# Performance work log

Hardware: AMD Instinct MI355X
Metric: run time of the kernel (lower is better)

Reference implementation:

```python
import jax, jax.numpy as jnp
import numpy as np

D_MODEL = 1024
NHEAD = 16
D_K = D_MODEL // NHEAD
EPS = 1e-5


def _layernorm(x, scale, bias):
    m = jnp.mean(x, axis=-1, keepdims=True)
    v = jnp.var(x, axis=-1, keepdims=True)
    return (x - m) * jax.lax.rsqrt(v + EPS) * scale + bias


def setup_inputs() -> dict:
    key = jax.random.key(0)
    ks = jax.random.split(key, 16)
    d, h = D_MODEL, 4 * D_MODEL
    s = 1.0 / np.sqrt(d)
    inp = {
        "x": jax.random.normal(ks[0], (2, 2048, d), dtype=jnp.float32),
        "Wq": jax.random.normal(ks[1], (d, d), dtype=jnp.float32) * s,
        "bq": jnp.zeros((d,), jnp.float32),
        "Wk": jax.random.normal(ks[2], (d, d), dtype=jnp.float32) * s,
        "bk": jnp.zeros((d,), jnp.float32),
        "Wv": jax.random.normal(ks[3], (d, d), dtype=jnp.float32) * s,
        "bv": jnp.zeros((d,), jnp.float32),
        "Wo": jax.random.normal(ks[4], (d, d), dtype=jnp.float32) * s,
        "bo": jnp.zeros((d,), jnp.float32),
        "ln1_scale": jnp.ones((d,), jnp.float32),
        "ln1_bias": jnp.zeros((d,), jnp.float32),
        "ln2_scale": jnp.ones((d,), jnp.float32),
        "ln2_bias": jnp.zeros((d,), jnp.float32),
        "W1": jax.random.normal(ks[5], (d, h), dtype=jnp.float32) * s,
        "b1": jnp.zeros((h,), jnp.float32),
        "W2": jax.random.normal(ks[6], (h, d), dtype=jnp.float32) * (1.0 / np.sqrt(h)),
        "b2": jnp.zeros((d,), jnp.float32),
    }
    return inp


def reference(x, Wq, bq, Wk, bk, Wv, bv, Wo, bo,
              ln1_scale, ln1_bias, ln2_scale, ln2_bias,
              W1, b1, W2, b2):
    batch, seq, d_model = x.shape
    # Faithful to original: q is viewed WITHOUT transpose (asymmetric vs k,v)
    q = (x @ Wq + bq).reshape(batch, NHEAD, seq, D_K)
    k = (x @ Wk + bk).reshape(batch, seq, NHEAD, D_K).transpose(0, 2, 1, 3)
    v = (x @ Wv + bv).reshape(batch, seq, NHEAD, D_K).transpose(0, 2, 1, 3)
    # scores: [B, H, S, S]
    scores = jnp.einsum('bhqd,bhkd->bhqk', q, k) / np.sqrt(D_K)
    attn = jax.nn.softmax(scores, axis=-1)
    o = jnp.einsum('bhqk,bhkd->bhqd', attn, v)  # [B,H,S,dk]
    o = o.transpose(0, 2, 1, 3).reshape(batch, seq, d_model)
    x = _layernorm(x + o @ Wo + bo, ln1_scale, ln1_bias)
    ff = jax.nn.relu(x @ W1 + b1) @ W2 + b2
    x = _layernorm(x + ff, ln2_scale, ln2_bias)
    return x
```

## Files before the change

### kernel.cpp

```cpp
#include <hip/hip_runtime.h>
#include <cstdint>

typedef __bf16 bf16x8 __attribute__((ext_vector_type(8)));
typedef float  floatx4 __attribute__((ext_vector_type(4)));

__device__ __forceinline__ unsigned short f2bf(float x) {
  union { float f; uint32_t u; } v; v.f = x;
  uint32_t r = (v.u + 0x7FFFu + ((v.u >> 16) & 1u)) >> 16;
  return (unsigned short)r;
}

__device__ __forceinline__ void async_copy16(const void* g, void* l) {
  __builtin_amdgcn_global_load_lds(
      (const __attribute__((address_space(1))) uint32_t*)g,
      (__attribute__((address_space(3))) uint32_t*)l, 16, 0, 0);
}

template<int OUT_BF16, int RELU>
__global__ __launch_bounds__(256, 2)
void gemm_bt_kernel(const unsigned short* __restrict__ A,
                    const unsigned short* __restrict__ Bt,
                    void* __restrict__ C, const float* __restrict__ bias,
                    int M, int N, int K, int Kper) {
  __shared__ __align__(16) unsigned short lA[128 * 32];
  __shared__ __align__(16) unsigned short lB[128 * 32];
  const int tid  = threadIdx.x;
  const int wave = tid >> 6;
  const int lane = tid & 63;

  const int gx = gridDim.x, gy = gridDim.y;
  int flat = blockIdx.y * gx + blockIdx.x;
  const int per = (gx * gy) >> 3;
  flat = (flat & 7) * per + (flat >> 3);
  const int sq = flat >> 6, inner = flat & 63;
  const int sqm = gy >> 3;
  const int m0 = ((sq % sqm) * 8 + (inner & 7)) * 128;
  const int n0 = ((sq / sqm) * 8 + (inner >> 3)) * 128;

  const int kz = blockIdx.z;
  const int wm = (wave >> 1) * 64;
  const int wn = (wave & 1) * 64;
  const int sa_row = lane >> 2;
  const int sa_k   = ((lane & 3) ^ ((lane >> 3) & 3)) * 8;
  const int fr = lane & 15;
  const int fq = lane >> 4;
  const int sw = (fr >> 1) & 3;

  floatx4 acc[4][4];
  #pragma unroll
  for (int i = 0; i < 4; ++i)
    #pragma unroll
    for (int j = 0; j < 4; ++j)
      acc[i][j] = (floatx4){0.f, 0.f, 0.f, 0.f};

  const int kIters = Kper >> 5;
  for (int kt = 0; kt < kIters; ++kt) {
    const int k0 = kz * Kper + (kt << 5);
    __syncthreads();
    #pragma unroll
    for (int j = 0; j < 2; ++j) {
      const int chunk = wave * 2 + j;
      const int row   = chunk * 16 + sa_row;
      async_copy16(A  + (size_t)(m0 + row) * K + (k0 + sa_k), &lA[chunk * 512]);
      async_copy16(Bt + (size_t)(n0 + row) * K + (k0 + sa_k), &lB[chunk * 512]);
    }
    asm volatile("s_waitcnt vmcnt(0)" ::: "memory");
    __syncthreads();
    bf16x8 af[4], bf[4];
    #pragma unroll
    for (int t = 0; t < 4; ++t) {
      af[t] = *(const bf16x8*)&lA[(wm + t * 16 + fr) * 32 + (fq ^ sw) * 8];
      bf[t] = *(const bf16x8*)&lB[(wn + t * 16 + fr) * 32 + (fq ^ sw) * 8];
    }
    #pragma unroll
    for (int mt = 0; mt < 4; ++mt)
      #pragma unroll
      for (int nt = 0; nt < 4; ++nt)
        acc[mt][nt] = __builtin_amdgcn_mfma_f32_16x16x32_bf16(af[mt], bf[nt], acc[mt][nt], 0, 0, 0);
  }

  const float* bp = (kz == 0) ? bias : nullptr;
  char* Cz = (char*)C + (size_t)kz * M * N * (OUT_BF16 ? 2 : 4);
  #pragma unroll
  for (int mt = 0; mt < 4; ++mt) {
    #pragma unroll
    for (int nt = 0; nt < 4; ++nt) {
      const int gn = n0 + wn + nt * 16 + fr;
      const float bv = bp ? bp[gn] : 0.f;
      #pragma unroll
      for (int r = 0; r < 4; ++r) {
        const int gm = m0 + wm + mt * 16 + fq * 4 + r;
        float v = acc[mt][nt][r] + bv;
        if (RELU) v = fmaxf(v, 0.f);
        if (OUT_BF16) ((unsigned short*)Cz)[(size_t)gm * N + gn] = f2bf(v);
        else          ((float*)Cz)[(size_t)gm * N + gn] = v;
      }
    }
  }
}

__global__ __launch_bounds__(256)
void repack_v_kernel(const unsigned short* __restrict__ X,
                     unsigned short* __restrict__ Vt) {
  const int bid = blockIdx.x;
  const int st = bid & 31, h = (bid >> 5) & 15, b = bid >> 9;
  const int bh = b * 16 + h;
  const int s0 = st * 64;
  const int t = threadIdx.x;
  const int sl = t >> 2;
  const int c  = (t & 3) * 16;
  __shared__ __align__(16) unsigned short vt[64][72];
  {
    const uint4* srcV = (const uint4*)(X + (size_t)(b * 2048 + s0 + sl) * 3072 + 2048 + h * 64 + c);
    uint4* dstL = (uint4*)&vt[sl][c];
    dstL[0] = srcV[0]; dstL[1] = srcV[1];
  }
  __syncthreads();
  const int d = t >> 2, c0 = (t & 3) * 16;
  unsigned short tmp[16];
  #pragma unroll
  for (int j = 0; j < 16; ++j) {
    const int chat = c0 + j;
    const int key = (chat & 3) * 16 + (chat >> 2);
    tmp[j] = vt[key][d];
  }
  uint4* dstV = (uint4*)(Vt + ((size_t)bh * 64 + d) * 2048 + s0 + c0);
  dstV[0] = *(uint4*)&tmp[0];
  dstV[1] = *(uint4*)&tmp[8];
}

__global__ __launch_bounds__(256, 4)
void flash_attn_kernel(const unsigned short* __restrict__ QKVb,
                       const unsigned short* __restrict__ Vt,
                       float* __restrict__ Opart, float* __restrict__ Lpart) {
  const int bid = blockIdx.x;
  const int qt = bid & 15, h = (bid >> 4) & 15, b = (bid >> 8) & 1, ksp = bid >> 9;
  const int bh = b * 16 + h;
  const int wave = threadIdx.x >> 6, lane = threadIdx.x & 63;
  const int fr = lane & 15, fq = lane >> 4;

  __shared__ __align__(16) unsigned short lK[64 * 64];
  __shared__ __align__(16) unsigned short lV[64 * 64];
  __shared__ __align__(16) unsigned short lP[4][32 * 72];

  const int q_base = qt * 128 + wave * 32;
  bf16x8 aq[2][2];
  #pragma unroll
  for (int g = 0; g < 2; ++g) {
    const int s2 = q_base + g * 16 + fr;
    const unsigned short* qp = QKVb + (size_t)(b * 2048 + h * 128 + (s2 >> 4)) * 3072
                             + (s2 & 15) * 64 + fq * 8;
    aq[g][0] = *(const bf16x8*)qp;
    aq[g][1] = *(const bf16x8*)(qp + 32);
  }
  floatx4 o_acc[2][4];
  #pragma unroll
  for (int g = 0; g < 2; ++g)
    #pragma unroll
    for (int nt = 0; nt < 4; ++nt) o_acc[g][nt] = (floatx4){0.f, 0.f, 0.f, 0.f};
  float lrow[2][4];
  #pragma unroll
  for (int g = 0; g < 2; ++g)
    #pragma unroll
    for (int r = 0; r < 4; ++r) lrow[g][r] = 0.f;

  const unsigned short* Kg = QKVb + 1024 + h * 64;
  const unsigned short* Vg = Vt + (size_t)bh * 64 * 2048;

  const int srow = lane >> 3;
  const int scol = ((lane & 7) ^ (lane >> 3)) * 8;
  const int sw = fr & 7;

  for (int kt = ksp * 16; kt < ksp * 16 + 16; ++kt) {
    __syncthreads();
    #pragma unroll
    for (int j = 0; j < 2; ++j) {
      const int ch = wave * 2 + j;
      const int krow = ch * 8 + srow;
      async_copy16(Kg + (size_t)(b * 2048 + kt * 64 + krow) * 3072 + scol, (char*)lK + ch * 1024);
      async_copy16(Vg + (size_t)krow * 2048 + kt * 64 + scol, (char*)lV + ch * 1024);
    }
    asm volatile("s_waitcnt vmcnt(0)" ::: "memory");
    __syncthreads();

    floatx4 s_acc[2][4];
    #pragma unroll
    for (int nt = 0; nt < 4; ++nt) {
      const int row = (nt * 16 + fr) * 64;
      bf16x8 bk0 = *(const bf16x8*)&lK[row + ((0 + fq) ^ sw) * 8];
      bf16x8 bk1 = *(const bf16x8*)&lK[row + ((4 + fq) ^ sw) * 8];
      #pragma unroll
      for (int g = 0; g < 2; ++g) {
        floatx4 acc = (floatx4){0.f, 0.f, 0.f, 0.f};
        acc = __builtin_amdgcn_mfma_f32_16x16x32_bf16(aq[g][0], bk0, acc, 0, 0, 0);
        acc = __builtin_amdgcn_mfma_f32_16x16x32_bf16(aq[g][1], bk1, acc, 0, 0, 0);
        s_acc[g][nt] = acc;
      }
    }
    #pragma unroll
    for (int g = 0; g < 2; ++g) {
      #pragma unroll
      for (int r = 0; r < 4; ++r) {
        const float p0 = __builtin_amdgcn_exp2f(s_acc[g][0][r] * 0.18033688f);
        const float p1 = __builtin_amdgcn_exp2f(s_acc[g][1][r] * 0.18033688f);
        const float p2 = __builtin_amdgcn_exp2f(s_acc[g][2][r] * 0.18033688f);
        const float p3 = __builtin_amdgcn_exp2f(s_acc[g][3][r] * 0.18033688f);
        lrow[g][r] += (p0 + p1) + (p2 + p3);
        union { float f; uint32_t u; } c0, c1, c2, c3;
        c0.f = p0; c1.f = p1; c2.f = p2; c3.f = p3;
        uint2 pk;
        pk.x = (c1.u & 0xffff0000u) | (c0.u >> 16);
        pk.y = (c3.u & 0xffff0000u) | (c2.u >> 16);
        *(uint2*)&lP[wave][(g * 16 + fq * 4 + r) * 72 + fr * 4] = pk;
      }
    }
    #pragma unroll
    for (int g = 0; g < 2; ++g) {
      #pragma unroll
      for (int kk = 0; kk < 2; ++kk) {
        bf16x8 ap = *(const bf16x8*)&lP[wave][(g * 16 + fr) * 72 + kk * 32 + fq * 8];
        #pragma unroll
        for (int nt = 0; nt < 4; ++nt) {
          bf16x8 bv = *(const bf16x8*)&lV[(nt * 16 + fr) * 64 + ((kk * 4 + fq) ^ sw) * 8];
          o_acc[g][nt] = __builtin_amdgcn_mfma_f32_16x16x32_bf16(ap, bv, o_acc[g][nt], 0, 0, 0);
        }
      }
    }
  }

  const size_t rbase = (size_t)ksp * 65536 + (size_t)bh * 2048 + q_base;
  #pragma unroll
  for (int g = 0; g < 2; ++g) {
    #pragma unroll
    for (int r = 0; r < 4; ++r) {
      float l = lrow[g][r];
      #pragma unroll
      for (int off = 1; off < 16; off <<= 1) l += __shfl_xor(l, off);
      if (fr == 0) Lpart[rbase + g * 16 + fq * 4 + r] = l;
    }
    #pragma unroll
    for (int nt = 0; nt < 4; ++nt)
      #pragma unroll
      for (int r = 0; r < 4; ++r)
        Opart[(rbase + g * 16 + fq * 4 + r) * 64 + nt * 16 + fr] = o_acc[g][nt][r];
  }
}

__global__ __launch_bounds__(256)
void attn_combine_kernel(const float* __restrict__ Opart, const float* __restrict__ Lpart,
                         unsigned short* __restrict__ O) {
  const int i = blockIdx.x * 256 + threadIdx.x;
  const int row = i >> 4;
  const int d4 = (i & 15) * 4;
  const float4 o0 = *(const float4*)&Opart[(size_t)row * 64 + d4];
  const float4 o1 = *(const float4*)&Opart[(size_t)(row + 65536) * 64 + d4];
  const float inv = 1.f / (Lpart[row] + Lpart[row + 65536]);
  const int bq = ((row >> 15) << 11) | (row & 2047);
  const int h = (row >> 11) & 15;
  ushort4 r;
  r.x = f2bf((o0.x + o1.x) * inv);
  r.y = f2bf((o0.y + o1.y) * inv);
  r.z = f2bf((o0.z + o1.z) * inv);
  r.w = f2bf((o0.w + o1.w) * inv);
  *(ushort4*)&O[(size_t)bq * 1024 + h * 64 + d4] = r;
}

__global__ __launch_bounds__(256)
void ln_kernel(const float* __restrict__ X, const float* __restrict__ R,
               const float* __restrict__ R2,
               const float* __restrict__ sc, const float* __restrict__ bi,
               float* __restrict__ outF, unsigned short* __restrict__ outB) {
  const int row = blockIdx.x;
  const int t = threadIdx.x;
  const size_t base = (size_t)row * 1024 + t * 4;
  float4 a  = *(const float4*)&X[base];
  const float4 rv = *(const float4*)&R[base];
  const float4 r2 = *(const float4*)&R2[base];
  a.x += rv.x + r2.x; a.y += rv.y + r2.y; a.z += rv.z + r2.z; a.w += rv.w + r2.w;
  float sum = (a.x + a.y) + (a.z + a.w);
  float sq  = (a.x * a.x + a.y * a.y) + (a.z * a.z + a.w * a.w);
  #pragma unroll
  for (int off = 32; off > 0; off >>= 1) {
    sum += __shfl_down(sum, off);
    sq  += __shfl_down(sq, off);
  }
  __shared__ float s1[4], s2a[4];
  const int wave = t >> 6, lane = t & 63;
  if (lane == 0) { s1[wave] = sum; s2a[wave] = sq; }
  __syncthreads();
  sum = (s1[0] + s1[1]) + (s1[2] + s1[3]);
  sq  = (s2a[0] + s2a[1]) + (s2a[2] + s2a[3]);
  const float mean = sum * (1.f / 1024.f);
  const float var  = sq * (1.f / 1024.f) - mean * mean;
  const float rstd = rsqrtf(var + 1e-5f);
  const float4 s = *(const float4*)&sc[t * 4];
  const float4 bb = *(const float4*)&bi[t * 4];
  float4 y;
  y.x = (a.x - mean) * rstd * s.x + bb.x;
  y.y = (a.y - mean) * rstd * s.y + bb.y;
  y.z = (a.z - mean) * rstd * s.z + bb.z;
  y.w = (a.w - mean) * rstd * s.w + bb.w;
  if (outF) *(float4*)&outF[base] = y;
  if (outB) {
    ushort4 ob; ob.x = f2bf(y.x); ob.y = f2bf(y.y); ob.z = f2bf(y.z); ob.w = f2bf(y.w);
    *(ushort4*)&outB[base] = ob;
  }
}

__global__ void transpose_all_kernel(const float* __restrict__ Wq, const float* __restrict__ Wk,
                                     const float* __restrict__ Wv, const float* __restrict__ Wo,
                                     const float* __restrict__ W1, const float* __restrict__ W2,
                                     unsigned short* __restrict__ Wqkvt, unsigned short* __restrict__ Wot,
                                     unsigned short* __restrict__ W1t, unsigned short* __restrict__ W2t) {
  const int id = blockIdx.x;
  const float* W; unsigned short* Wt; int K, N, tile;
  if (id < 4096) {
    const int w = id >> 10; tile = id & 1023; K = 1024; N = 1024;
    if (w == 0)      { W = Wq; Wt = Wqkvt; }
    else if (w == 1) { W = Wk; Wt = Wqkvt + 1024 * 1024; }
    else if (w == 2) { W = Wv; Wt = Wqkvt + 2048 * 1024; }
    else             { W = Wo; Wt = Wot; }
  } else if (id < 8192) { tile = id - 4096; W = W1; Wt = W1t; K = 1024; N = 4096; }
  else                  { tile = id - 8192; W = W2; Wt = W2t; K = 4096; N = 1024; }
  const int tilesX = N >> 5;
  const int bx = (tile & (tilesX - 1)) * 32;
  const int by = (tile / tilesX) * 32;
  __shared__ float tl[32][33];
  const int tx = threadIdx.x, ty = threadIdx.y;
  #pragma unroll
  for (int i = ty; i < 32; i += 8)
    tl[i][tx] = W[(size_t)(by + i) * N + bx + tx];
  __syncthreads();
  #pragma unroll
  for (int i = ty; i < 32; i += 8)
    Wt[(size_t)(bx + i) * K + by + tx] = f2bf(tl[tx][i]);
}

__global__ void cast_bf16_kernel(const float* __restrict__ in,
                                 unsigned short* __restrict__ out, int n4) {
  const int i = blockIdx.x * 256 + threadIdx.x;
  if (i < n4) {
    float4 v = ((const float4*)in)[i];
    ushort4 o;
    o.x = f2bf(v.x); o.y = f2bf(v.y); o.z = f2bf(v.z); o.w = f2bf(v.w);
    ((ushort4*)out)[i] = o;
  }
}

__global__ void concat3_kernel(const float* __restrict__ a, const float* __restrict__ b,
                               const float* __restrict__ c, float* __restrict__ out) {
  int i = blockIdx.x * 256 + threadIdx.x;
  if (i < 1024) out[i] = a[i];
  else if (i < 2048) out[i] = b[i - 1024];
  else if (i < 3072) out[i] = c[i - 2048];
}

extern "C" void kernel_launch(void* const* d_in, const int* in_sizes, int n_in,
                              void* d_out, int out_size, void* d_ws, size_t ws_size,
                              hipStream_t stream) {
  const float* x    = (const float*)d_in[0];
  const float* Wq   = (const float*)d_in[1];
  const float* bq   = (const float*)d_in[2];
  const float* Wk   = (const float*)d_in[3];
  const float* bk   = (const float*)d_in[4];
  const float* Wv   = (const float*)d_in[5];
  const float* bv   = (const float*)d_in[6];
  const float* Wo   = (const float*)d_in[7];
  const float* bo   = (const float*)d_in[8];
  const float* ln1s = (const float*)d_in[9];
  const float* ln1b = (const float*)d_in[10];
  const float* ln2s = (const float*)d_in[11];
  const float* ln2b = (const float*)d_in[12];
  const float* W1   = (const float*)d_in[13];
  const float* b1   = (const float*)d_in[14];
  const float* W2   = (const float*)d_in[15];
  const float* b2   = (const float*)d_in[16];
  float* out = (float*)d_out;

  char* ws = (char*)d_ws;
  const size_t MB = 1u << 20;
  unsigned short* QKVb = (unsigned short*)(ws + 0);
  float*          t1   = (float*)(ws + 0);
  unsigned short* ffh  = (unsigned short*)(ws + 0);
  unsigned short* Vt   = (unsigned short*)(ws + 32 * MB);
  unsigned short* Ob   = (unsigned short*)(ws + 40 * MB);
  float*          ff   = (float*)(ws + 32 * MB);
  float*          Opart= (float*)(ws + 48 * MB);
  unsigned short* xb   = (unsigned short*)(ws + 48 * MB);
  unsigned short* Wqkvt= (unsigned short*)(ws + 56 * MB);
  float*          x1   = (float*)(ws + 64 * MB);
  float*          Lpart= (float*)(ws + 80 * MB);
  unsigned short* Wot  = (unsigned short*)(ws + 81 * MB);
  unsigned short* W1t  = (unsigned short*)(ws + 83 * MB);
  unsigned short* W2t  = (unsigned short*)(ws + 91 * MB);
  float*          bqkv = (float*)(ws + 99 * MB);
  unsigned short* x1b  = (unsigned short*)(ws + 100 * MB);

  cast_bf16_kernel<<<4096, 256, 0, stream>>>(x, xb, 1048576);
  transpose_all_kernel<<<12288, dim3(32, 8), 0, stream>>>(Wq, Wk, Wv, Wo, W1, W2,
                                                          Wqkvt, Wot, W1t, W2t);
  concat3_kernel<<<12, 256, 0, stream>>>(bq, bk, bv, bqkv);

  gemm_bt_kernel<1, 0><<<dim3(24, 32, 1), 256, 0, stream>>>(xb, Wqkvt, QKVb, bqkv, 4096, 3072, 1024, 1024);
  repack_v_kernel<<<1024, 256, 0, stream>>>(QKVb, Vt);
  flash_attn_kernel<<<1024, 256, 0, stream>>>(QKVb, Vt, Opart, Lpart);
  attn_combine_kernel<<<4096, 256, 0, stream>>>(Opart, Lpart, Ob);
  gemm_bt_kernel<0, 0><<<dim3(8, 32, 2), 256, 0, stream>>>(Ob, Wot, t1, bo, 4096, 1024, 1024, 512);
  ln_kernel<<<4096, 256, 0, stream>>>(x, t1, t1 + 4096 * 1024, ln1s, ln1b, x1, x1b);
  gemm_bt_kernel<1, 1><<<dim3(32, 32, 1), 256, 0, stream>>>(x1b, W1t, ffh, b1, 4096, 4096, 1024, 1024);
  gemm_bt_kernel<0, 0><<<dim3(8, 32, 2), 256, 0, stream>>>(ffh, W2t, ff, b2, 4096, 1024, 4096, 2048);
  ln_kernel<<<4096, 256, 0, stream>>>(x1, ff, ff + 4096 * 1024, ln2s, ln2b, out, nullptr);

  (void)in_sizes; (void)n_in; (void)out_size; (void)ws_size;
}
```

Before: 370.5 us.

## Double-buffer LDS tiles in GEMM to overlap async global loads with MFMA

Adds a second pair of LDS buffers to the bf16 GEMM so the next K-tile is prefetched via global_load_lds while the current tile feeds the MFMAs. Partial vmcnt waits and raw s_barrier replace the full drain and __syncthreads each iteration. It also precomputes the per-thread row pointers. The cost is double the LDS per block, which may limit occupancy, and the loop assumes an even kIters.

```diff
diff --git a/kernel.cpp b/kernel.cpp
--- a/kernel.cpp
+++ b/kernel.cpp
@@ -22,8 +22,10 @@
                     const unsigned short* __restrict__ Bt,
                     void* __restrict__ C, const float* __restrict__ bias,
                     int M, int N, int K, int Kper) {
-  __shared__ __align__(16) unsigned short lA[128 * 32];
-  __shared__ __align__(16) unsigned short lB[128 * 32];
+  __shared__ __align__(16) unsigned short l0A[128 * 32];
+  __shared__ __align__(16) unsigned short l0B[128 * 32];
+  __shared__ __align__(16) unsigned short l1A[128 * 32];
+  __shared__ __align__(16) unsigned short l1B[128 * 32];
   const int tid  = threadIdx.x;
   const int wave = tid >> 6;
   const int lane = tid & 63;
@@ -46,6 +48,13 @@
   const int fq = lane >> 4;
   const int sw = (fr >> 1) & 3;
 
+  const int r0 = (wave * 2 + 0) * 16 + sa_row;
+  const int r1 = (wave * 2 + 1) * 16 + sa_row;
+  const unsigned short* A0 = A  + (size_t)(m0 + r0) * K + kz * Kper + sa_k;
+  const unsigned short* A1 = A  + (size_t)(m0 + r1) * K + kz * Kper + sa_k;
+  const unsigned short* B0 = Bt + (size_t)(n0 + r0) * K + kz * Kper + sa_k;
+  const unsigned short* B1 = Bt + (size_t)(n0 + r1) * K + kz * Kper + sa_k;
+
   floatx4 acc[4][4];
   #pragma unroll
   for (int i = 0; i < 4; ++i)
@@ -53,31 +62,54 @@
     for (int j = 0; j < 4; ++j)
       acc[i][j] = (floatx4){0.f, 0.f, 0.f, 0.f};
 
+  const int c0 = (wave * 2 + 0) * 512;
+  const int c1 = (wave * 2 + 1) * 512;
+
+#define PREFETCH(kt, LA, LB)                                   \
+  do {                                                         \
+    const int koff = (kt) << 5;                                \
+    async_copy16(A0 + koff, &(LA)[c0]);                        \
+    async_copy16(A1 + koff, &(LA)[c1]);                        \
+    async_copy16(B0 + koff, &(LB)[c0]);                        \
+    async_copy16(B1 + koff, &(LB)[c1]);                        \
+  } while (0)
+
+#define COMPUTE(LA, LB)                                                        \
+  do {                                                                         \
+    bf16x8 af[4], bf[4];                                                       \
+    _Pragma("unroll")                                                          \
+    for (int t = 0; t < 4; ++t) {                                              \
+      af[t] = *(const bf16x8*)&(LA)[(wm + t * 16 + fr) * 32 + (fq ^ sw) * 8];  \
+      bf[t] = *(const bf16x8*)&(LB)[(wn + t * 16 + fr) * 32 + (fq ^ sw) * 8];  \
+    }                                                                          \
+    _Pragma("unroll")                                                          \
+    for (int mt = 0; mt < 4; ++mt)                                             \
+      _Pragma("unroll")                                                        \
+      for (int nt = 0; nt < 4; ++nt)                                           \
+        acc[mt][nt] = __builtin_amdgcn_mfma_f32_16x16x32_bf16(af[mt], bf[nt],  \
+                                                              acc[mt][nt], 0, 0, 0); \
+  } while (0)
+
   const int kIters = Kper >> 5;
-  for (int kt = 0; kt < kIters; ++kt) {
-    const int k0 = kz * Kper + (kt << 5);
-    __syncthreads();
-    #pragma unroll
-    for (int j = 0; j < 2; ++j) {
-      const int chunk = wave * 2 + j;
-      const int row   = chunk * 16 + sa_row;
-      async_copy16(A  + (size_t)(m0 + row) * K + (k0 + sa_k), &lA[chunk * 512]);
-      async_copy16(Bt + (size_t)(n0 + row) * K + (k0 + sa_k), &lB[chunk * 512]);
-    }
-    asm volatile("s_waitcnt vmcnt(0)" ::: "memory");
-    __syncthreads();
-    bf16x8 af[4], bf[4];
-    #pragma unroll
-    for (int t = 0; t < 4; ++t) {
-      af[t] = *(const bf16x8*)&lA[(wm + t * 16 + fr) * 32 + (fq ^ sw) * 8];
-      bf[t] = *(const bf16x8*)&lB[(wn + t * 16 + fr) * 32 + (fq ^ sw) * 8];
-    }
-    #pragma unroll
-    for (int mt = 0; mt < 4; ++mt)
-      #pragma unroll
-      for (int nt = 0; nt < 4; ++nt)
-        acc[mt][nt] = __builtin_amdgcn_mfma_f32_16x16x32_bf16(af[mt], bf[nt], acc[mt][nt], 0, 0, 0);
-  }
+  PREFETCH(0, l0A, l0B);
+  for (int kt = 0; kt < kIters; kt += 2) {
+    PREFETCH(kt + 1, l1A, l1B);
+    asm volatile("s_waitcnt vmcnt(4)" ::: "memory");
+    asm volatile("s_barrier" ::: "memory");
+    COMPUTE(l0A, l0B);
+    asm volatile("s_barrier" ::: "memory");
+    if (kt + 2 < kIters) {
+      PREFETCH(kt + 2, l0A, l0B);
+      asm volatile("s_waitcnt vmcnt(4)" ::: "memory");
+    } else {
+      asm volatile("s_waitcnt vmcnt(0)" ::: "memory");
+    }
+    asm volatile("s_barrier" ::: "memory");
+    COMPUTE(l1A, l1B);
+    asm volatile("s_barrier" ::: "memory");
+  }
+#undef PREFETCH
+#undef COMPUTE
 
   const float* bp = (kz == 0) ? bias : nullptr;
   char* Cz = (char*)C + (size_t)kz * M * N * (OUT_BF16 ? 2 : 4);
@@ -116,15 +148,15 @@
     dstL[0] = srcV[0]; dstL[1] = srcV[1];
   }
   __syncthreads();
-  const int d = t >> 2, c0 = (t & 3) * 16;
+  const int d = t >> 2, cc = (t & 3) * 16;
   unsigned short tmp[16];
   #pragma unroll
   for (int j = 0; j < 16; ++j) {
-    const int chat = c0 + j;
+    const int chat = cc + j;
     const int key = (chat & 3) * 16 + (chat >> 2);
     tmp[j] = vt[key][d];
   }
-  uint4* dstV = (uint4*)(Vt + ((size_t)bh * 64 + d) * 2048 + s0 + c0);
+  uint4* dstV = (uint4*)(Vt + ((size_t)bh * 64 + d) * 2048 + s0 + cc);
   dstV[0] = *(uint4*)&tmp[0];
   dstV[1] = *(uint4*)&tmp[8];
 }
```

Result: faster. 362.6 us (-2.1%).
